# Kernel tuning notes

Hardware: AMD Instinct MI355X
Metric: run time of the kernel (lower is better)

The kernel has to match this reference:

```python
import jax, jax.numpy as jnp
import numpy as np

N_NODES = 100000
N_EDGES = 1600000
N_FEAT = 128
H_CH = 64
N_GRAPHS = 4096
N_LAY = 3


def _gcn_conv(x, W, bias, src, dst, dinv):
    # GCNConv with self-loops: out = D^{-1/2}(A+I)D^{-1/2} (x W) + bias
    h = x @ W  # [N, out]
    coef = (dinv[src] * dinv[dst])[:, None]  # [E, 1]
    agg = jax.ops.segment_sum(h[src] * coef, dst, num_segments=N_NODES)
    agg = agg + h * (dinv * dinv)[:, None]  # self-loop term
    return agg + bias


def setup_inputs() -> dict:
    key = jax.random.key(0)
    ks = jax.random.split(key, 12)
    x = jax.random.normal(ks[0], (N_NODES, N_FEAT), dtype=jnp.float32)
    e_idx = jax.random.randint(ks[1], (2, N_EDGES), 0, N_NODES, dtype=jnp.int32)
    b = jnp.sort(jax.random.randint(ks[2], (N_NODES,), 0, N_GRAPHS, dtype=jnp.int32))
    s = 0.05
    w0 = jax.random.normal(ks[3], (N_FEAT, H_CH), dtype=jnp.float32) * s
    b0 = jax.random.normal(ks[4], (H_CH,), dtype=jnp.float32) * s
    convW = jax.random.normal(ks[5], (N_LAY - 1, H_CH, H_CH), dtype=jnp.float32) * s
    convB = jax.random.normal(ks[6], (N_LAY - 1, H_CH), dtype=jnp.float32) * s
    skipW = jax.random.normal(ks[7], (N_LAY - 1, H_CH, H_CH), dtype=jnp.float32) * s
    skipB = jax.random.normal(ks[8], (N_LAY - 1, H_CH), dtype=jnp.float32) * s
    lin1W = jax.random.normal(ks[9], (H_CH, H_CH // 2), dtype=jnp.float32) * s
    lin1b = jnp.zeros((H_CH // 2,), dtype=jnp.float32)
    lin2W = jax.random.normal(ks[10], (H_CH // 2, 1), dtype=jnp.float32) * s
    lin2b = jnp.zeros((1,), dtype=jnp.float32)
    return {"x": x, "e_idx": e_idx, "b": b, "w0": w0, "b0": b0,
            "convW": convW, "convB": convB, "skipW": skipW, "skipB": skipB,
            "lin1W": lin1W, "lin1b": lin1b, "lin2W": lin2W, "lin2b": lin2b}


def reference(x, e_idx, b, w0, b0, convW, convB, skipW, skipB, lin1W, lin1b, lin2W, lin2b):
    src, dst = e_idx[0], e_idx[1]
    # degree (with self-loop) computed on destination nodes, as in PyG GCNConv
    deg = jax.ops.segment_sum(jnp.ones((N_EDGES,), x.dtype), dst, num_segments=N_NODES) + 1.0
    dinv = jax.lax.rsqrt(deg)

    h = jax.nn.relu(_gcn_conv(x, w0, b0, src, dst, dinv))  # dropout: eval mode identity
    for i in range(N_LAY - 1):
        h_n = jax.nn.relu(_gcn_conv(h, convW[i], convB[i], src, dst, dinv))
        h_s = h @ skipW[i] + skipB[i]
        h = h_n + h_s

    # global mean pool over graph ids
    sums = jax.ops.segment_sum(h, b, num_segments=N_GRAPHS)
    cnts = jax.ops.segment_sum(jnp.ones((N_NODES,), x.dtype), b, num_segments=N_GRAPHS)
    pooled = sums / jnp.maximum(cnts, 1.0)[:, None]  # [G, H]

    out = jax.nn.relu(pooled @ lin1W + lin1b)
    return out @ lin2W + lin2b  # [G, 1]
```

## Files before the change

### kernel.cpp

```cpp
#include <hip/hip_runtime.h>
#include <hip/hip_fp16.h>

#define NN 100000
#define NE 1600000
#define NF 128
#define H  64
#define NG 4096

#define NBK 512
#define BKN 196
#define CAP 4096
#define NBLK_BIN 256
#define CHUNK ((NE + NBLK_BIN - 1) / NBLK_BIN)

typedef unsigned long long u64;
typedef unsigned int u32;

__device__ inline u32 packh2(float x, float y) {
  __half2 h = __floats2half2_rn(x, y);
  return *reinterpret_cast<u32*>(&h);
}
__device__ inline float2 unpackh2(u32 u) {
  __half2 h = *reinterpret_cast<__half2*>(&u);
  return __half22float2(h);
}

__global__ __launch_bounds__(256) void k_bin(const int* __restrict__ src,
                                             const int* __restrict__ dst,
                                             int* __restrict__ bcur,
                                             u32* __restrict__ ebuf) {
  __shared__ int d_s[CHUNK];
  __shared__ int bcnt[NBK], bpos[NBK];
  const int e0 = blockIdx.x * CHUNK;
  const int e1 = min(e0 + CHUNK, NE);
  for (int i = threadIdx.x; i < NBK; i += 256) bcnt[i] = 0;
  __syncthreads();
  for (int e = e0 + threadIdx.x; e < e1; e += 256) {
    const int d = dst[e];
    d_s[e - e0] = d;
    atomicAdd(&bcnt[d / BKN], 1);
  }
  __syncthreads();
  for (int i = threadIdx.x; i < NBK; i += 256) {
    const int c = bcnt[i];
    if (c) bpos[i] = i * CAP + atomicAdd(&bcur[i], c);
  }
  __syncthreads();
  for (int e = e0 + threadIdx.x; e < e1; e += 256) {
    const int d = d_s[e - e0];
    const int bk = d / BKN;
    const int pos = atomicAdd(&bpos[bk], 1);
    ebuf[pos] = ((u32)(d - bk * BKN) << 17) | (u32)src[e];
  }
}

__global__ __launch_bounds__(256) void k_csr(const int* __restrict__ bcur,
                                             const u32* __restrict__ ebuf,
                                             int* __restrict__ row_ptr,
                                             int* __restrict__ cnt,
                                             float* __restrict__ dinv,
                                             int* __restrict__ csr_src) {
  __shared__ u32 eb_s[CAP];
  __shared__ int deg[256], sc[256], cur[256];
  const int bk = blockIdx.x;
  const int nlo = bk * BKN;
  if (nlo >= NN) return;
  const int nloc = min(BKN, NN - nlo);
  const int cntE = bcur[bk];
  const int t = threadIdx.x;
  for (int e = t; e < cntE; e += 256) eb_s[e] = ebuf[(size_t)bk * CAP + e];
  deg[t] = 0;
  __syncthreads();
  for (int e = t; e < cntE; e += 256) atomicAdd(&deg[eb_s[e] >> 17], 1);
  __syncthreads();
  sc[t] = deg[t];
  __syncthreads();
  for (int off = 1; off < 256; off <<= 1) {
    const int add = (t >= off) ? sc[t - off] : 0;
    __syncthreads();
    sc[t] += add;
    __syncthreads();
  }
  const int excl = bk * CAP + sc[t] - deg[t];
  if (t < nloc) {
    row_ptr[nlo + t] = excl;
    cnt[nlo + t] = deg[t];
    dinv[nlo + t] = 1.0f / sqrtf((float)deg[t] + 1.0f);
  }
  cur[t] = excl;
  __syncthreads();
  for (int oct = 0; oct < 8; ++oct) {
    for (int e = t; e < cntE; e += 256) {
      const u32 ent = eb_s[e];
      const int s = (int)(ent & 0x1ffffu);
      if (((s >> 14) & 7) == oct) {
        const int pos = atomicAdd(&cur[ent >> 17], 1);
        csr_src[pos] = s;
      }
    }
    __syncthreads();
  }
}

#define TSTR 388
template <int CI, bool SK>
__global__ __launch_bounds__(256) void k_gemm(const float* __restrict__ in,
                                              const float* __restrict__ W,
                                              const float* __restrict__ Ws,
                                              const float* __restrict__ bs,
                                              const float* __restrict__ dinv,
                                              u32* __restrict__ out16,
                                              float* __restrict__ outS) {
  __shared__ float wt[CI * 64];
  __shared__ float wsl[SK ? 64 * 64 : 1];
  __shared__ float tin[8 * TSTR];
  for (int i = threadIdx.x; i < CI * 64; i += 256) wt[i] = W[i];
  if (SK)
    for (int i = threadIdx.x; i < 64 * 64; i += 256) wsl[i] = Ws[i];

  const int row0 = blockIdx.x * 256;
  const int rg = threadIdx.x >> 3;
  const int cg = threadIdx.x & 7;
  float acc[8][8];
  float sacc[SK ? 8 : 1][SK ? 8 : 1];
#pragma unroll
  for (int i = 0; i < 8; ++i)
#pragma unroll
    for (int j = 0; j < 8; ++j) acc[i][j] = 0.0f;
  if (SK) {
#pragma unroll
    for (int i = 0; i < 8; ++i)
#pragma unroll
      for (int j = 0; j < 8; ++j) sacc[i][j] = bs[cg * 8 + j];
  }

  const int kk = (threadIdx.x & 1) * 4;
  const int rr = threadIdx.x >> 1;
  for (int k0 = 0; k0 < CI; k0 += 8) {
    __syncthreads();
#pragma unroll
    for (int s = 0; s < 2; ++s) {
      const int r = s * 128 + rr;
      const int rowc = min(row0 + r, NN - 1);
      const float4 v = *(const float4*)(in + (size_t)rowc * CI + k0 + kk);
      const int base = (r >> 3) * 12 + (r & 7);
      tin[(kk + 0) * TSTR + base] = v.x;
      tin[(kk + 1) * TSTR + base] = v.y;
      tin[(kk + 2) * TSTR + base] = v.z;
      tin[(kk + 3) * TSTR + base] = v.w;
    }
    __syncthreads();
#pragma unroll
    for (int k = 0; k < 8; ++k) {
      const float4 a0 = *(const float4*)&tin[k * TSTR + rg * 12];
      const float4 a1 = *(const float4*)&tin[k * TSTR + rg * 12 + 4];
      const float af[8] = {a0.x, a0.y, a0.z, a0.w, a1.x, a1.y, a1.z, a1.w};
      const float4 b0 = *(const float4*)&wt[(k0 + k) * 64 + cg * 8];
      const float4 b1 = *(const float4*)&wt[(k0 + k) * 64 + cg * 8 + 4];
      const float bf[8] = {b0.x, b0.y, b0.z, b0.w, b1.x, b1.y, b1.z, b1.w};
#pragma unroll
      for (int i = 0; i < 8; ++i)
#pragma unroll
        for (int j = 0; j < 8; ++j) acc[i][j] = fmaf(af[i], bf[j], acc[i][j]);
      if (SK) {
        const float4 c0 = *(const float4*)&wsl[(k0 + k) * 64 + cg * 8];
        const float4 c1 = *(const float4*)&wsl[(k0 + k) * 64 + cg * 8 + 4];
        const float cf[8] = {c0.x, c0.y, c0.z, c0.w, c1.x, c1.y, c1.z, c1.w};
#pragma unroll
        for (int i = 0; i < 8; ++i)
#pragma unroll
          for (int j = 0; j < 8; ++j) sacc[i][j] = fmaf(af[i], cf[j], sacc[i][j]);
      }
    }
  }
#pragma unroll
  for (int i = 0; i < 8; ++i) {
    const int row = row0 + rg * 8 + i;
    if (row < NN) {
      const float dv = dinv[row];
      u32 o[4];
#pragma unroll
      for (int j = 0; j < 4; ++j)
        o[j] = packh2(acc[i][2 * j] * dv, acc[i][2 * j + 1] * dv);
      *(uint4*)&out16[(size_t)row * 32 + cg * 4] =
          make_uint4(o[0], o[1], o[2], o[3]);
      if (SK) {
        float* sp = outS + (size_t)row * 64 + cg * 8;
        *(float4*)(sp) = make_float4(sacc[i][0], sacc[i][1], sacc[i][2], sacc[i][3]);
        *(float4*)(sp + 4) = make_float4(sacc[i][4], sacc[i][5], sacc[i][6], sacc[i][7]);
      }
    }
  }
}

template <bool ADD_S>
__global__ __launch_bounds__(256) void k_agg(const u32* __restrict__ hw16,
                                             const float* __restrict__ hs,
                                             const int* __restrict__ csr_src,
                                             const int* __restrict__ row_ptr,
                                             const int* __restrict__ cnt,
                                             const float* __restrict__ dinv,
                                             const float* __restrict__ bias,
                                             float* __restrict__ h) {
  const int lane = threadIdx.x & 31;
  const int half = (threadIdx.x >> 5) & 1;
  const int wv = threadIdx.x >> 6;
  const int n = (blockIdx.x * 4 + wv) * 2 + half;
  const int beg = row_ptr[n];
  const int deg = cnt[n];
  const int dm = max(deg, __shfl_xor(deg, 32));
  float2 a[8];
#pragma unroll
  for (int k = 0; k < 8; ++k) a[k] = make_float2(0.0f, 0.0f);
  int i = 0;

#define GSTEP(NK)                                                             \
  {                                                                           \
    int p[NK];                                                                \
    u32 uv[NK];                                                               \
    _Pragma("unroll") for (int k = 0; k < NK; ++k) {                          \
      int e = i + k;                                                          \
      e = e < deg ? e : deg - 1;                                              \
      e = e > 0 ? e : 0;                                                      \
      p[k] = __builtin_nontemporal_load(&csr_src[beg + e]);                   \
    }                                                                         \
    _Pragma("unroll") for (int k = 0; k < NK; ++k)                            \
        uv[k] = hw16[(size_t)p[k] * 32 + lane];                               \
    _Pragma("unroll") for (int k = 0; k < NK; ++k) {                          \
      const float2 f = unpackh2(uv[k]);                                       \
      const bool ok = (i + k) < deg;                                          \
      a[k & 7].x += ok ? f.x : 0.0f;                                          \
      a[k & 7].y += ok ? f.y : 0.0f;                                          \
    }                                                                         \
    i += NK;                                                                  \
  }

  while (i + 16 <= dm) GSTEP(16)
  if (i + 8 <= dm) GSTEP(8)
  if (i + 4 <= dm) GSTEP(4)
  if (i + 2 <= dm) GSTEP(2)
  if (i < dm) GSTEP(1)
#undef GSTEP

  float2 t0 = make_float2(a[0].x + a[1].x, a[0].y + a[1].y);
  float2 t1 = make_float2(a[2].x + a[3].x, a[2].y + a[3].y);
  float2 t2 = make_float2(a[4].x + a[5].x, a[4].y + a[5].y);
  float2 t3 = make_float2(a[6].x + a[7].x, a[6].y + a[7].y);
  float2 acc = make_float2((t0.x + t1.x) + (t2.x + t3.x),
                           (t0.y + t1.y) + (t2.y + t3.y));
  const float2 self = unpackh2(hw16[(size_t)n * 32 + lane]);
  const float dv = dinv[n];
  const float2 brc = *(const float2*)&bias[2 * lane];
  float2 r;
  r.x = fmaxf((acc.x + self.x) * dv + brc.x, 0.0f);
  r.y = fmaxf((acc.y + self.y) * dv + brc.y, 0.0f);
  if (ADD_S) {
    const float2 s = *(const float2*)&hs[(size_t)n * 64 + 2 * lane];
    r.x += s.x;
    r.y += s.y;
  }
  *(float2*)&h[(size_t)n * 64 + 2 * lane] = r;
}

__global__ __launch_bounds__(256) void k_pool(const float* __restrict__ h,
                                              const int* __restrict__ b,
                                              float* __restrict__ pool,
                                              float* __restrict__ cnt) {
  const int col = threadIdx.x & 63;
  const int wv  = threadIdx.x >> 6;
  const int node0 = (blockIdx.x * 4 + wv) * 64;
  if (node0 >= NN) return;
  const int node1 = min(node0 + 64, NN);
  int gcur = b[node0];
  float acc = 0.f;
  float run = 0.f;
  for (int n = node0; n < node1; ++n) {
    const int g = b[n];
    if (g != gcur) {
      atomicAdd(&pool[(size_t)gcur * 64 + col], acc);
      if (col == 0) atomicAdd(&cnt[gcur], run);
      gcur = g; acc = 0.f; run = 0.f;
    }
    acc += h[(size_t)n * 64 + col];
    run += 1.f;
  }
  atomicAdd(&pool[(size_t)gcur * 64 + col], acc);
  if (col == 0) atomicAdd(&cnt[gcur], run);
}

__global__ __launch_bounds__(64) void k_head(const float* __restrict__ pool,
                                             const float* __restrict__ cnt,
                                             const float* __restrict__ lin1W,
                                             const float* __restrict__ lin1b,
                                             const float* __restrict__ lin2W,
                                             const float* __restrict__ lin2b,
                                             float* __restrict__ out) {
  const int g = blockIdx.x;
  const int lane = threadIdx.x;
  const float c = fmaxf(cnt[g], 1.0f);
  float r = 0.f;
  if (lane < 32) {
    float s = lin1b[lane];
    const float* p = pool + (size_t)g * 64;
#pragma unroll 8
    for (int ci = 0; ci < 64; ++ci) s = fmaf(p[ci] / c, lin1W[ci * 32 + lane], s);
    r = fmaxf(s, 0.0f) * lin2W[lane];
  }
  for (int off = 32; off > 0; off >>= 1) r += __shfl_down(r, off, 64);
  if (lane == 0) out[g] = r + lin2b[0];
}

extern "C" void kernel_launch(void* const* d_in, const int* in_sizes, int n_in,
                              void* d_out, int out_size, void* d_ws, size_t ws_size,
                              hipStream_t stream) {
  const float* x     = (const float*)d_in[0];
  const int*   src   = (const int*)d_in[1];
  const int*   dst   = ((const int*)d_in[1]) + NE;
  const int*   b     = (const int*)d_in[2];
  const float* w0    = (const float*)d_in[3];
  const float* b0    = (const float*)d_in[4];
  const float* convW = (const float*)d_in[5];
  const float* convB = (const float*)d_in[6];
  const float* skipW = (const float*)d_in[7];
  const float* skipB = (const float*)d_in[8];
  const float* lin1W = (const float*)d_in[9];
  const float* lin1b = (const float*)d_in[10];
  const float* lin2W = (const float*)d_in[11];
  const float* lin2b = (const float*)d_in[12];
  float* out = (float*)d_out;

  char* w = (char*)d_ws;
  const size_t NPAD = 102400;
  int*   cnt     = (int*)w;                  w += NPAD * 4;
  float* dinv    = (float*)w;                w += NPAD * 4;
  int*   row_ptr = (int*)w;                  w += NPAD * 4;
  int*   bcur    = (int*)w;                  w += 1024 * 4;
  int*   csr_src = (int*)w;                  w += (size_t)NBK * CAP * 4;
  char*  big     = w;                        w += (size_t)NN * 32 * 4;
  float* hA      = (float*)w;                w += (size_t)NN * 64 * 4;
  float* hS      = (float*)w;                w += (size_t)NN * 64 * 4;
  float* pool    = (float*)w;                w += (size_t)NG * 64 * 4;
  float* pcnt    = (float*)w;                w += (size_t)NG * 4;
  u32* ebuf = (u32*)big;
  u32* hw16 = (u32*)big;

  hipMemsetAsync(bcur, 0, NBK * sizeof(int), stream);
  k_bin<<<NBLK_BIN, 256, 0, stream>>>(src, dst, bcur, ebuf);
  k_csr<<<NBK, 256, 0, stream>>>(bcur, ebuf, row_ptr, cnt, dinv, csr_src);

  const int GT = (NN + 255) / 256;

  k_gemm<NF, false><<<GT, 256, 0, stream>>>(x, w0, nullptr, nullptr, dinv,
                                            hw16, nullptr);
  k_agg<false><<<12500, 256, 0, stream>>>(hw16, nullptr, csr_src, row_ptr, cnt,
                                          dinv, b0, hA);
  for (int i = 0; i < 2; ++i) {
    k_gemm<H, true><<<GT, 256, 0, stream>>>(hA, convW + (size_t)i * H * H,
                                            skipW + (size_t)i * H * H,
                                            skipB + (size_t)i * H, dinv, hw16, hS);
    k_agg<true><<<12500, 256, 0, stream>>>(hw16, hS, csr_src, row_ptr, cnt,
                                           dinv, convB + (size_t)i * H, hA);
  }

  hipMemsetAsync(pool, 0, ((size_t)NG * 64 + NG) * sizeof(float), stream);
  k_pool<<<(NN / 256) + 1, 256, 0, stream>>>(hA, b, pool, pcnt);
  k_head<<<NG, 64, 0, stream>>>(pool, pcnt, lin1W, lin1b, lin2W, lin2b, out);
}
```

Before: 330.2 us.

## Sort nodes by degree and aggregate with four nodes per wavefront

```diff
diff --git a/kernel.cpp b/kernel.cpp
--- a/kernel.cpp
+++ b/kernel.cpp
@@ -95,11 +95,59 @@
       const int s = (int)(ent & 0x1ffffu);
       if (((s >> 14) & 7) == oct) {
         const int pos = atomicAdd(&cur[ent >> 17], 1);
-        csr_src[pos] = s;
+        csr_src[pos] = s << 4;
       }
     }
     __syncthreads();
   }
+  for (int e = cntE + t; e < min(cntE + 64, CAP); e += 256)
+    csr_src[bk * CAP + e] = 0;
+}
+
+__global__ __launch_bounds__(256) void k_obin(const int* __restrict__ cnt,
+                                              int* __restrict__ gcur) {
+  __shared__ int lh[64];
+  const int t = threadIdx.x;
+  if (t < 64) lh[t] = 0;
+  __syncthreads();
+  const int n = blockIdx.x * 256 + t;
+  if (n < NN) atomicAdd(&lh[min(cnt[n], 63)], 1);
+  __syncthreads();
+  if (t < 64 && lh[t]) atomicAdd(&gcur[t], lh[t]);
+}
+
+__global__ __launch_bounds__(64) void k_oscan(int* __restrict__ gcur) {
+  __shared__ int sh[64];
+  const int t = threadIdx.x;
+  const int v = gcur[t];
+  sh[t] = v;
+  __syncthreads();
+  for (int off = 1; off < 64; off <<= 1) {
+    const int a = (t >= off) ? sh[t - off] : 0;
+    __syncthreads();
+    sh[t] += a;
+    __syncthreads();
+  }
+  gcur[t] = sh[t] - v;
+}
+
+__global__ __launch_bounds__(256) void k_oscat(const int* __restrict__ cnt,
+                                               int* __restrict__ gcur,
+                                               int* __restrict__ order) {
+  __shared__ int lh[64], lo[64];
+  const int t = threadIdx.x;
+  if (t < 64) lh[t] = 0;
+  __syncthreads();
+  const int n = blockIdx.x * 256 + t;
+  int bin = 0, loc = 0;
+  if (n < NN) {
+    bin = min(cnt[n], 63);
+    loc = atomicAdd(&lh[bin], 1);
+  }
+  __syncthreads();
+  if (t < 64 && lh[t]) lo[t] = atomicAdd(&gcur[t], lh[t]);
+  __syncthreads();
+  if (n < NN) order[lo[bin] + loc] = n;
 }
 
 #define TSTR 388
@@ -201,65 +249,63 @@
                                              const int* __restrict__ cnt,
                                              const float* __restrict__ dinv,
                                              const float* __restrict__ bias,
+                                             const int* __restrict__ order,
                                              float* __restrict__ h) {
-  const int lane = threadIdx.x & 31;
-  const int half = (threadIdx.x >> 5) & 1;
-  const int wv = threadIdx.x >> 6;
-  const int n = (blockIdx.x * 4 + wv) * 2 + half;
+  const int lane = threadIdx.x & 63;
+  const int grp  = lane >> 4;
+  const int cl   = lane & 15;
+  const int wv   = threadIdx.x >> 6;
+  const int slot = (blockIdx.x * 4 + wv) * 4 + grp;
+  const int n = order[slot];
   const int beg = row_ptr[n];
   const int deg = cnt[n];
-  const int dm = max(deg, __shfl_xor(deg, 32));
-  float2 a[8];
-#pragma unroll
-  for (int k = 0; k < 8; ++k) a[k] = make_float2(0.0f, 0.0f);
+  const int d1 = max(deg, __shfl_xor(deg, 16));
+  const int dmax = max(d1, __shfl_xor(d1, 32));
+  const u64* hw64 = (const u64*)hw16;
+  float4 acc = make_float4(0.f, 0.f, 0.f, 0.f);
   int i = 0;
 
 #define GSTEP(NK)                                                             \
   {                                                                           \
     int p[NK];                                                                \
-    u32 uv[NK];                                                               \
+    uint2 uv[NK];                                                             \
+    _Pragma("unroll") for (int k = 0; k < NK; ++k)                            \
+        p[k] = __builtin_nontemporal_load(&csr_src[beg + i + k]);             \
+    _Pragma("unroll") for (int k = 0; k < NK; ++k)                            \
+        uv[k] = *(const uint2*)&hw64[(size_t)(p[k] + cl)];                    \
     _Pragma("unroll") for (int k = 0; k < NK; ++k) {                          \
-      int e = i + k;                                                          \
-      e = e < deg ? e : deg - 1;                                              \
-      e = e > 0 ? e : 0;                                                      \
-      p[k] = __builtin_nontemporal_load(&csr_src[beg + e]);                   \
-    }                                                                         \
-    _Pragma("unroll") for (int k = 0; k < NK; ++k)                            \
-        uv[k] = hw16[(size_t)p[k] * 32 + lane];                               \
-    _Pragma("unroll") for (int k = 0; k < NK; ++k) {                          \
-      const float2 f = unpackh2(uv[k]);                                       \
-      const bool ok = (i + k) < deg;                                          \
-      a[k & 7].x += ok ? f.x : 0.0f;                                          \
-      a[k & 7].y += ok ? f.y : 0.0f;                                          \
+      const float m = ((i + k) < deg) ? 1.0f : 0.0f;                          \
+      const float2 f0 = unpackh2(uv[k].x);                                    \
+      const float2 f1 = unpackh2(uv[k].y);                                    \
+      acc.x = fmaf(f0.x, m, acc.x);                                           \
+      acc.y = fmaf(f0.y, m, acc.y);                                           \
+      acc.z = fmaf(f1.x, m, acc.z);                                           \
+      acc.w = fmaf(f1.y, m, acc.w);                                           \
     }                                                                         \
     i += NK;                                                                  \
   }
 
-  while (i + 16 <= dm) GSTEP(16)
-  if (i + 8 <= dm) GSTEP(8)
-  if (i + 4 <= dm) GSTEP(4)
-  if (i + 2 <= dm) GSTEP(2)
-  if (i < dm) GSTEP(1)
+  while (i + 8 <= dmax) GSTEP(8)
+  if (i + 4 <= dmax) GSTEP(4)
+  if (i + 2 <= dmax) GSTEP(2)
+  if (i < dmax) GSTEP(1)
 #undef GSTEP
 
-  float2 t0 = make_float2(a[0].x + a[1].x, a[0].y + a[1].y);
-  float2 t1 = make_float2(a[2].x + a[3].x, a[2].y + a[3].y);
-  float2 t2 = make_float2(a[4].x + a[5].x, a[4].y + a[5].y);
-  float2 t3 = make_float2(a[6].x + a[7].x, a[6].y + a[7].y);
-  float2 acc = make_float2((t0.x + t1.x) + (t2.x + t3.x),
-                           (t0.y + t1.y) + (t2.y + t3.y));
-  const float2 self = unpackh2(hw16[(size_t)n * 32 + lane]);
+  const uint2 sv = *(const uint2*)&hw64[(size_t)n * 16 + cl];
+  const float2 s0 = unpackh2(sv.x);
+  const float2 s1 = unpackh2(sv.y);
   const float dv = dinv[n];
-  const float2 brc = *(const float2*)&bias[2 * lane];
-  float2 r;
-  r.x = fmaxf((acc.x + self.x) * dv + brc.x, 0.0f);
-  r.y = fmaxf((acc.y + self.y) * dv + brc.y, 0.0f);
+  const float4 brc = *(const float4*)&bias[cl * 4];
+  float4 r;
+  r.x = fmaxf((acc.x + s0.x) * dv + brc.x, 0.0f);
+  r.y = fmaxf((acc.y + s0.y) * dv + brc.y, 0.0f);
+  r.z = fmaxf((acc.z + s1.x) * dv + brc.z, 0.0f);
+  r.w = fmaxf((acc.w + s1.y) * dv + brc.w, 0.0f);
   if (ADD_S) {
-    const float2 s = *(const float2*)&hs[(size_t)n * 64 + 2 * lane];
-    r.x += s.x;
-    r.y += s.y;
-  }
-  *(float2*)&h[(size_t)n * 64 + 2 * lane] = r;
+    const float4 s = *(const float4*)&hs[(size_t)n * 64 + cl * 4];
+    r.x += s.x; r.y += s.y; r.z += s.z; r.w += s.w;
+  }
+  *(float4*)&h[(size_t)n * 64 + cl * 4] = r;
 }
 
 __global__ __launch_bounds__(256) void k_pool(const float* __restrict__ h,
@@ -334,8 +380,10 @@
   int*   cnt     = (int*)w;                  w += NPAD * 4;
   float* dinv    = (float*)w;                w += NPAD * 4;
   int*   row_ptr = (int*)w;                  w += NPAD * 4;
+  int*   order   = (int*)w;                  w += NPAD * 4;
   int*   bcur    = (int*)w;                  w += 1024 * 4;
-  int*   csr_src = (int*)w;                  w += (size_t)NBK * CAP * 4;
+  int*   gcur    = (int*)w;                  w += 1024 * 4;
+  int*   csr_src = (int*)w;                  w += (size_t)NBK * CAP * 4 + 4096;
   char*  big     = w;                        w += (size_t)NN * 32 * 4;
   float* hA      = (float*)w;                w += (size_t)NN * 64 * 4;
   float* hS      = (float*)w;                w += (size_t)NN * 64 * 4;
@@ -345,21 +393,26 @@
   u32* hw16 = (u32*)big;
 
   hipMemsetAsync(bcur, 0, NBK * sizeof(int), stream);
+  hipMemsetAsync(gcur, 0, 64 * sizeof(int), stream);
   k_bin<<<NBLK_BIN, 256, 0, stream>>>(src, dst, bcur, ebuf);
   k_csr<<<NBK, 256, 0, stream>>>(bcur, ebuf, row_ptr, cnt, dinv, csr_src);
+  const int OB = (NN + 255) / 256;
+  k_obin<<<OB, 256, 0, stream>>>(cnt, gcur);
+  k_oscan<<<1, 64, 0, stream>>>(gcur);
+  k_oscat<<<OB, 256, 0, stream>>>(cnt, gcur, order);
 
   const int GT = (NN + 255) / 256;
 
   k_gemm<NF, false><<<GT, 256, 0, stream>>>(x, w0, nullptr, nullptr, dinv,
                                             hw16, nullptr);
-  k_agg<false><<<12500, 256, 0, stream>>>(hw16, nullptr, csr_src, row_ptr, cnt,
-                                          dinv, b0, hA);
+  k_agg<false><<<6250, 256, 0, stream>>>(hw16, nullptr, csr_src, row_ptr, cnt,
+                                         dinv, b0, order, hA);
   for (int i = 0; i < 2; ++i) {
     k_gemm<H, true><<<GT, 256, 0, stream>>>(hA, convW + (size_t)i * H * H,
                                             skipW + (size_t)i * H * H,
                                             skipB + (size_t)i * H, dinv, hw16, hS);
-    k_agg<true><<<12500, 256, 0, stream>>>(hw16, hS, csr_src, row_ptr, cnt,
-                                           dinv, convB + (size_t)i * H, hA);
+    k_agg<true><<<6250, 256, 0, stream>>>(hw16, hS, csr_src, row_ptr, cnt,
+                                          dinv, convB + (size_t)i * H, order, hA);
   }
 
   hipMemsetAsync(pool, 0, ((size_t)NG * 64 + NG) * sizeof(float), stream);
```

Result: faster. 323.3 us (-2.1%).
